# Optimization experiments

Measured on AMD Instinct MI355X. Metric: run time of the kernel, lower is better.

The kernel has to match this reference:

```python
import jax, jax.numpy as jnp
import numpy as np

DIM = 768
NUM_HEADS = 16
HEAD_DIM = DIM // NUM_HEADS
SCALE = HEAD_DIM ** -0.5


def setup_inputs() -> dict:
    key = jax.random.key(0)
    ks = jax.random.split(key, 9)
    B, S = 4, 2048
    init = 1.0 / np.sqrt(DIM)
    x = jax.random.normal(ks[0], (B, S, DIM), dtype=jnp.float32)
    Wq = jax.random.uniform(ks[1], (DIM, DIM), jnp.float32, -init, init)
    bq = jax.random.uniform(ks[2], (DIM,), jnp.float32, -init, init)
    Wk = jax.random.uniform(ks[3], (DIM, DIM), jnp.float32, -init, init)
    bk = jax.random.uniform(ks[4], (DIM,), jnp.float32, -init, init)
    Wv = jax.random.uniform(ks[5], (DIM, DIM), jnp.float32, -init, init)
    bv = jax.random.uniform(ks[6], (DIM,), jnp.float32, -init, init)
    Wo = jax.random.uniform(ks[7], (DIM, DIM), jnp.float32, -init, init)
    bo = jax.random.uniform(ks[8], (DIM,), jnp.float32, -init, init)
    return {"x": x, "Wq": Wq, "bq": bq, "Wk": Wk, "bk": bk,
            "Wv": Wv, "bv": bv, "Wo": Wo, "bo": bo}


def reference(x, Wq, bq, Wk, bk, Wv, bv, Wo, bo):
    B, S, D = x.shape
    H, Hd = NUM_HEADS, HEAD_DIM
    # Linear layers (torch Linear: y = x @ W^T + b); split heads -> [B,H,S,Hd]
    q = (x @ Wq.T + bq).reshape(B, S, H, Hd).transpose(0, 2, 1, 3)
    k = (x @ Wk.T + bk).reshape(B, S, H, Hd).transpose(0, 2, 1, 3)
    v = (x @ Wv.T + bv).reshape(B, S, H, Hd).transpose(0, 2, 1, 3)
    scores = jnp.einsum('bhqd,bhkd->bhqk', q, k) * SCALE  # [B,H,S,S]
    attn = jax.nn.softmax(scores, axis=-1)
    # dropout is identity in eval mode
    out = jnp.einsum('bhqk,bhkd->bhqd', attn, v)
    out = out.transpose(0, 2, 1, 3).reshape(B, S, D)
    return out @ Wo.T + bo
```

## Files before the change

kernel.cpp:

```cpp
#include <hip/hip_runtime.h>

typedef __bf16 bf16_t;
typedef bf16_t bf16x8 __attribute__((ext_vector_type(8)));
typedef _Float16 f16_t;
typedef __fp16 hf16x2 __attribute__((ext_vector_type(2)));
typedef f16_t f16x8 __attribute__((ext_vector_type(8)));
typedef float floatx4 __attribute__((ext_vector_type(4)));
typedef float floatx16 __attribute__((ext_vector_type(16)));

#define S_LEN 2048
#define DIM 768
#define NH 16
#define HD 48
#define HDP 64
#define BHEADS 64
#define ATT_SCALE 0.14433756729740643f
#define W_ELEMS (DIM * DIM)

typedef unsigned short u16;
typedef unsigned int u32;

__device__ __forceinline__ u16 f2b(float f) {
  union { float f; u32 i; } z; z.f = f;
  u32 i = z.i;
  return (u16)((i + 0x7fffu + ((i >> 16) & 1u)) >> 16);
}
__device__ __forceinline__ u32 pack2(float a, float b) {
  return (u32)f2b(a) | ((u32)f2b(b) << 16);
}
__device__ __forceinline__ u32 pkrtz2(float a, float b) {
  union { hf16x2 h; u32 u; } z;
  z.h = __builtin_amdgcn_cvt_pkrtz(a, b);
  return z.u;
}
__device__ __forceinline__ void pl32swap(u32& a, u32& b) {
  asm("v_permlane32_swap_b32 %0, %1" : "+v"(a), "+v"(b));
}

__global__ __launch_bounds__(256) void cvt_f32_bf16(
    const float* __restrict__ src, u16* __restrict__ dst)
{
  int idx = blockIdx.x * 256 + threadIdx.x;
  const float4* s = (const float4*)src;
  float4 a = s[idx * 2], b = s[idx * 2 + 1];
  *(uint4*)&dst[(size_t)idx * 8] =
      make_uint4(pack2(a.x, a.y), pack2(a.z, a.w), pack2(b.x, b.y), pack2(b.z, b.w));
}

__global__ __launch_bounds__(256) void cvt_weights(
    const float* __restrict__ w0, const float* __restrict__ w1,
    const float* __restrict__ w2, const float* __restrict__ w3,
    u16* __restrict__ dst)
{
  const float* srcs[4] = {w0, w1, w2, w3};
  const float* src = srcs[blockIdx.y];
  u16* d = dst + (size_t)blockIdx.y * W_ELEMS;
  int idx = blockIdx.x * 256 + threadIdx.x;
  const float4* s = (const float4*)src;
  float4 a = s[idx * 2], b = s[idx * 2 + 1];
  *(uint4*)&d[(size_t)idx * 8] =
      make_uint4(pack2(a.x, a.y), pack2(a.z, a.w), pack2(b.x, b.y), pack2(b.z, b.w));
}

template<int OMODE>
__global__ __launch_bounds__(256) void gemm_bt(
    const u16* __restrict__ A, const u16* __restrict__ W,
    const float* __restrict__ bias, void* __restrict__ outv, float scale)
{
  __shared__ __attribute__((aligned(16))) u16 smem[8704];
  u16 (*As)[40] = (u16(*)[40])smem;
  u16 (*Bs)[40] = (u16(*)[40])(smem + 5120);

  const int tid = threadIdx.x;
  const int w = tid >> 6, lane = tid & 63, lo = lane & 15, quad = lane >> 4;
  const int bm = blockIdx.x & 63, bn = blockIdx.x >> 6;
  const int m0 = bm * 128, n0 = bn * 64;

  floatx4 acc[2][4];
#pragma unroll
  for (int mi = 0; mi < 2; mi++)
#pragma unroll
    for (int ni = 0; ni < 4; ni++) acc[mi][ni] = (floatx4){0.f, 0.f, 0.f, 0.f};

  for (int k0 = 0; k0 < DIM; k0 += 32) {
#pragma unroll
    for (int it = 0; it < 2; ++it) {
      int c = tid + it * 256;
      int r = c >> 2, cc = c & 3;
      *(uint4*)&As[r][cc * 8] = *(const uint4*)&A[(size_t)(m0 + r) * DIM + k0 + cc * 8];
    }
    {
      int r = tid >> 2, cc = tid & 3;
      *(uint4*)&Bs[r][cc * 8] = *(const uint4*)&W[(size_t)(n0 + r) * DIM + k0 + cc * 8];
    }
    __syncthreads();
    bf16x8 af[2], bfr[4];
#pragma unroll
    for (int mi = 0; mi < 2; mi++) af[mi] = *(const bf16x8*)&As[w * 32 + mi * 16 + lo][quad * 8];
#pragma unroll
    for (int ni = 0; ni < 4; ni++) bfr[ni] = *(const bf16x8*)&Bs[ni * 16 + lo][quad * 8];
#pragma unroll
    for (int mi = 0; mi < 2; mi++)
#pragma unroll
      for (int ni = 0; ni < 4; ni++)
        acc[mi][ni] = __builtin_amdgcn_mfma_f32_16x16x32_bf16(af[mi], bfr[ni], acc[mi][ni], 0, 0, 0);
    __syncthreads();
  }

  if constexpr (OMODE == 2) {
    u16 (*T)[136] = (u16(*)[136])smem;
    u16* out = (u16*)outv;
#pragma unroll
    for (int mi = 0; mi < 2; mi++)
#pragma unroll
      for (int ni = 0; ni < 4; ni++) {
        int col = ni * 16 + lo;
        float bb = bias[n0 + col];
        float v0 = acc[mi][ni][0] + bb, v1 = acc[mi][ni][1] + bb;
        float v2 = acc[mi][ni][2] + bb, v3 = acc[mi][ni][3] + bb;
        *(uint2*)&T[col][w * 32 + mi * 16 + quad * 4] =
            make_uint2(pkrtz2(v0, v1), pkrtz2(v2, v3));
      }
    __syncthreads();
    const int b = m0 >> 11, s0 = m0 & 2047;
#pragma unroll
    for (int it = 0; it < 4; ++it) {
      int ch = tid + it * 256;
      int col = ch >> 4, sc = ch & 15;
      int gcol = n0 + col;
      int h = gcol / HD, d = gcol - h * HD;
      size_t dst = ((size_t)(b * NH + h) * HDP + d) * S_LEN + s0 + sc * 8;
      *(uint4*)&out[dst] = *(const uint4*)&T[col][sc * 8];
    }
    return;
  }

#pragma unroll
  for (int mi = 0; mi < 2; mi++)
#pragma unroll
    for (int ni = 0; ni < 4; ni++)
#pragma unroll
      for (int r = 0; r < 4; r++) {
        int row = m0 + w * 32 + mi * 16 + quad * 4 + r;
        int col = n0 + ni * 16 + lo;
        float v = (acc[mi][ni][r] + bias[col]) * scale;
        if constexpr (OMODE == 1) {
          ((float*)outv)[(size_t)row * DIM + col] = v;
        } else {
          int b = row >> 11, s = row & 2047;
          int h = col / HD, d = col - h * HD;
          ((u16*)outv)[((size_t)((b * NH + h) * S_LEN + s)) * HDP + d] = f2b(v);
        }
      }
}

#define STG_LOAD(k0n) do {                                                     \
  _Pragma("unroll")                                                            \
  for (int it = 0; it < 3; ++it) {                                             \
    int c = tid + it * 256;                                                    \
    if (c < 384) {                                                             \
      int r = c / 6, cc = c - r * 6;                                           \
      stg[it] = *(const uint4*)&K[base + (size_t)((k0n) + r) * HDP + cc * 8];  \
    } else {                                                                   \
      int c2 = c - 384, r = c2 >> 3, cc = c2 & 7;                              \
      stg[it] = *(const uint4*)&V[base + (size_t)r * S_LEN + (k0n) + cc * 8];  \
    }                                                                          \
  }                                                                            \
} while (0)

#define STG_WRITE(bufi) do {                                                   \
  _Pragma("unroll")                                                            \
  for (int it = 0; it < 3; ++it) {                                             \
    int c = tid + it * 256;                                                    \
    if (c < 384) {                                                             \
      int r = c / 6, cc = c - r * 6;                                           \
      *(uint4*)&Ks[bufi][r][cc * 8] = stg[it];                                 \
    } else {                                                                   \
      int c2 = c - 384, r = c2 >> 3, cc = c2 & 7;                              \
      *(uint4*)&Vt[bufi][r][cc * 8] = stg[it];                                 \
    }                                                                          \
  }                                                                            \
} while (0)

__global__ __launch_bounds__(256, 2) void attn_kernel(
    const u16* __restrict__ Q, const u16* __restrict__ K,
    const u16* __restrict__ V, u16* __restrict__ O)
{
  __shared__ __attribute__((aligned(16))) u16 Ks[2][64][56];
  __shared__ __attribute__((aligned(16))) u16 Vt[2][64][72];

  const int tid = threadIdx.x;
  const int w = tid >> 6, lane = tid & 63, l31 = lane & 31, hi = lane >> 5;
  const int q0 = blockIdx.x * 256;
  const int bh = blockIdx.y;
  const size_t base = (size_t)bh * S_LEN * HDP;

  bf16x8 qf[2][3];
#pragma unroll
  for (int t = 0; t < 2; t++)
#pragma unroll
    for (int ks = 0; ks < 3; ks++)
      qf[t][ks] = *(const bf16x8*)
          &Q[base + (size_t)(q0 + w * 64 + t * 32 + l31) * HDP + ks * 16 + hi * 8];

  floatx16 oacc[2][2];
#pragma unroll
  for (int t = 0; t < 2; t++)
#pragma unroll
    for (int nd = 0; nd < 2; nd++)
#pragma unroll
      for (int r = 0; r < 16; r++) oacc[t][nd][r] = 0.f;

  float l_lane[2] = {0.f, 0.f};

  uint4 stg[3];
  STG_LOAD(0);
  STG_WRITE(0);

  for (int ti = 0; ti < 32; ++ti) {
    const int cur = ti & 1;
    if (ti < 31) STG_LOAD((ti + 1) * 64);
    __syncthreads();

    bf16x8 ak[2][3];
#pragma unroll
    for (int na = 0; na < 2; na++)
#pragma unroll
      for (int ks = 0; ks < 3; ks++)
        ak[na][ks] = *(const bf16x8*)&Ks[cur][na * 32 + l31][ks * 16 + hi * 8];

    u32 pk[2][2][8];
#pragma unroll
    for (int t = 0; t < 2; t++) {
      floatx16 s0, s1;
#pragma unroll
      for (int r = 0; r < 16; r++) { s0[r] = 0.f; s1[r] = 0.f; }
#pragma unroll
      for (int ks = 0; ks < 3; ks++) {
        s0 = __builtin_amdgcn_mfma_f32_32x32x16_bf16(ak[0][ks], qf[t][ks], s0, 0, 0, 0);
        s1 = __builtin_amdgcn_mfma_f32_32x32x16_bf16(ak[1][ks], qf[t][ks], s1, 0, 0, 0);
      }
#pragma unroll
      for (int m = 0; m < 8; m++) {
        float a0 = __expf(s0[2 * m]), a1 = __expf(s0[2 * m + 1]);
        float b0 = __expf(s1[2 * m]), b1 = __expf(s1[2 * m + 1]);
        l_lane[t] += (a0 + a1) + (b0 + b1);
        pk[t][0][m] = pkrtz2(a0, a1);
        pk[t][1][m] = pkrtz2(b0, b1);
      }
    }

#pragma unroll
    for (int kt = 0; kt < 4; kt++) {
      f16x8 bv0 = *(const f16x8*)&Vt[cur][l31][kt * 16 + hi * 8];
      f16x8 bv1 = *(const f16x8*)&Vt[cur][32 + l31][kt * 16 + hi * 8];
      const int na = kt >> 1, k4 = (kt & 1) * 4;
#pragma unroll
      for (int t = 0; t < 2; t++) {
        u32 w0 = pk[t][na][k4 + 0], w2 = pk[t][na][k4 + 2];
        u32 w1 = pk[t][na][k4 + 1], w3 = pk[t][na][k4 + 3];
        pl32swap(w0, w2);
        pl32swap(w1, w3);
        union { u32 u[4]; f16x8 f; } af;
        af.u[0] = w0; af.u[1] = w1; af.u[2] = w2; af.u[3] = w3;
        oacc[t][0] = __builtin_amdgcn_mfma_f32_32x32x16_f16(af.f, bv0, oacc[t][0], 0, 0, 0);
        oacc[t][1] = __builtin_amdgcn_mfma_f32_32x32x16_f16(af.f, bv1, oacc[t][1], 0, 0, 0);
      }
    }

    if (ti < 31) STG_WRITE(cur ^ 1);
  }

  const int b = bh >> 4, h = bh & 15;
  float lt_full[2];
#pragma unroll
  for (int t = 0; t < 2; t++)
    lt_full[t] = l_lane[t] + __shfl_xor(l_lane[t], 32);
#pragma unroll
  for (int t = 0; t < 2; t++) {
#pragma unroll
    for (int r = 0; r < 16; r++) {
      int q_local = (r & 3) + 8 * (r >> 2) + 4 * hi;
      float l_r = __shfl(lt_full[t], q_local);
      float inv = 1.f / l_r;
      int q = q0 + w * 64 + t * 32 + q_local;
      size_t rowbase = ((size_t)(b * S_LEN + q)) * DIM + h * HD;
      O[rowbase + l31] = f2b(oacc[t][0][r] * inv);
      if (l31 < 16) O[rowbase + 32 + l31] = f2b(oacc[t][1][r] * inv);
    }
  }
}

extern "C" void kernel_launch(void* const* d_in, const int* in_sizes, int n_in,
                              void* d_out, int out_size, void* d_ws, size_t ws_size,
                              hipStream_t stream)
{
  const float* x  = (const float*)d_in[0];
  const float* Wq = (const float*)d_in[1];
  const float* bq = (const float*)d_in[2];
  const float* Wk = (const float*)d_in[3];
  const float* bk = (const float*)d_in[4];
  const float* Wv = (const float*)d_in[5];
  const float* bv = (const float*)d_in[6];
  const float* Wo = (const float*)d_in[7];
  const float* bo = (const float*)d_in[8];

  u16* ws   = (u16*)d_ws;
  const size_t qkv_elems = (size_t)BHEADS * S_LEN * HDP;
  u16* q_ws = ws;
  u16* k_ws = q_ws + qkv_elems;
  u16* v_ws = k_ws + qkv_elems;
  u16* x_bf = v_ws + qkv_elems;
  u16* a_ws = x_bf;
  u16* w_bf = x_bf + (size_t)8192 * DIM;

  cvt_f32_bf16<<<dim3(3072), dim3(256), 0, stream>>>(x, x_bf);
  cvt_weights<<<dim3(288, 4), dim3(256), 0, stream>>>(Wq, Wk, Wv, Wo, w_bf);
  u16* wq_bf = w_bf;
  u16* wk_bf = w_bf + (size_t)W_ELEMS;
  u16* wv_bf = w_bf + (size_t)2 * W_ELEMS;
  u16* wo_bf = w_bf + (size_t)3 * W_ELEMS;

  gemm_bt<0><<<dim3(768), dim3(256), 0, stream>>>(x_bf, wq_bf, bq, q_ws, ATT_SCALE);
  gemm_bt<0><<<dim3(768), dim3(256), 0, stream>>>(x_bf, wk_bf, bk, k_ws, 1.0f);
  gemm_bt<2><<<dim3(768), dim3(256), 0, stream>>>(x_bf, wv_bf, bv, v_ws, 1.0f);
  attn_kernel<<<dim3(S_LEN / 256, BHEADS), dim3(256), 0, stream>>>(q_ws, k_ws, v_ws, a_ws);
  gemm_bt<1><<<dim3(768), dim3(256), 0, stream>>>(a_ws, wo_bf, bo, d_out, 1.0f);
}
```

Measured before the change: 292.1 us.

## Halve attention query tile, raise occupancy, and remap blocks per XCD

Each attention block now handles 128 queries (32 per wave) instead of 256, so the grid grows from 512 to 1024 blocks and launch bounds move from 2 to 4 blocks per SM. A flat 1D grid is remapped so consecutive blocks on the same XCD share a head, which keeps that head's K/V in the XCD's L2. The aim is more concurrent waves to hide the exp/MFMA latency and better cache locality. The cost is twice as many K/V tile loads per query and less MFMA reuse of each K/V LDS fragment.

```diff
diff --git a/kernel.cpp b/kernel.cpp
--- a/kernel.cpp
+++ b/kernel.cpp
@@ -182,7 +182,7 @@
   }                                                                            \
 } while (0)
 
-__global__ __launch_bounds__(256, 2) void attn_kernel(
+__global__ __launch_bounds__(256, 4) void attn_kernel(
     const u16* __restrict__ Q, const u16* __restrict__ K,
     const u16* __restrict__ V, u16* __restrict__ O)
 {
@@ -191,27 +191,25 @@
 
   const int tid = threadIdx.x;
   const int w = tid >> 6, lane = tid & 63, l31 = lane & 31, hi = lane >> 5;
-  const int q0 = blockIdx.x * 256;
-  const int bh = blockIdx.y;
+  const int flat = blockIdx.x;
+  const int xcd = flat & 7, sub = flat >> 3;
+  const int bh = xcd * 8 + (sub >> 4);
+  const int q0 = (sub & 15) * 128;
   const size_t base = (size_t)bh * S_LEN * HDP;
 
-  bf16x8 qf[2][3];
-#pragma unroll
-  for (int t = 0; t < 2; t++)
-#pragma unroll
-    for (int ks = 0; ks < 3; ks++)
-      qf[t][ks] = *(const bf16x8*)
-          &Q[base + (size_t)(q0 + w * 64 + t * 32 + l31) * HDP + ks * 16 + hi * 8];
-
-  floatx16 oacc[2][2];
-#pragma unroll
-  for (int t = 0; t < 2; t++)
-#pragma unroll
-    for (int nd = 0; nd < 2; nd++)
-#pragma unroll
-      for (int r = 0; r < 16; r++) oacc[t][nd][r] = 0.f;
-
-  float l_lane[2] = {0.f, 0.f};
+  bf16x8 qf[3];
+#pragma unroll
+  for (int ks = 0; ks < 3; ks++)
+    qf[ks] = *(const bf16x8*)
+        &Q[base + (size_t)(q0 + w * 32 + l31) * HDP + ks * 16 + hi * 8];
+
+  floatx16 oacc[2];
+#pragma unroll
+  for (int nd = 0; nd < 2; nd++)
+#pragma unroll
+    for (int r = 0; r < 16; r++) oacc[nd][r] = 0.f;
+
+  float l_lane = 0.f;
 
   uint4 stg[3];
   STG_LOAD(0);
@@ -229,24 +227,23 @@
       for (int ks = 0; ks < 3; ks++)
         ak[na][ks] = *(const bf16x8*)&Ks[cur][na * 32 + l31][ks * 16 + hi * 8];
 
-    u32 pk[2][2][8];
-#pragma unroll
-    for (int t = 0; t < 2; t++) {
+    u32 pk[2][8];
+    {
       floatx16 s0, s1;
 #pragma unroll
       for (int r = 0; r < 16; r++) { s0[r] = 0.f; s1[r] = 0.f; }
 #pragma unroll
       for (int ks = 0; ks < 3; ks++) {
-        s0 = __builtin_amdgcn_mfma_f32_32x32x16_bf16(ak[0][ks], qf[t][ks], s0, 0, 0, 0);
-        s1 = __builtin_amdgcn_mfma_f32_32x32x16_bf16(ak[1][ks], qf[t][ks], s1, 0, 0, 0);
+        s0 = __builtin_amdgcn_mfma_f32_32x32x16_bf16(ak[0][ks], qf[ks], s0, 0, 0, 0);
+        s1 = __builtin_amdgcn_mfma_f32_32x32x16_bf16(ak[1][ks], qf[ks], s1, 0, 0, 0);
       }
 #pragma unroll
       for (int m = 0; m < 8; m++) {
         float a0 = __expf(s0[2 * m]), a1 = __expf(s0[2 * m + 1]);
         float b0 = __expf(s1[2 * m]), b1 = __expf(s1[2 * m + 1]);
-        l_lane[t] += (a0 + a1) + (b0 + b1);
-        pk[t][0][m] = pkrtz2(a0, a1);
-        pk[t][1][m] = pkrtz2(b0, b1);
+        l_lane += (a0 + a1) + (b0 + b1);
+        pk[0][m] = pkrtz2(a0, a1);
+        pk[1][m] = pkrtz2(b0, b1);
       }
     }
 
@@ -255,39 +252,30 @@
       f16x8 bv0 = *(const f16x8*)&Vt[cur][l31][kt * 16 + hi * 8];
       f16x8 bv1 = *(const f16x8*)&Vt[cur][32 + l31][kt * 16 + hi * 8];
       const int na = kt >> 1, k4 = (kt & 1) * 4;
-#pragma unroll
-      for (int t = 0; t < 2; t++) {
-        u32 w0 = pk[t][na][k4 + 0], w2 = pk[t][na][k4 + 2];
-        u32 w1 = pk[t][na][k4 + 1], w3 = pk[t][na][k4 + 3];
-        pl32swap(w0, w2);
-        pl32swap(w1, w3);
-        union { u32 u[4]; f16x8 f; } af;
-        af.u[0] = w0; af.u[1] = w1; af.u[2] = w2; af.u[3] = w3;
-        oacc[t][0] = __builtin_amdgcn_mfma_f32_32x32x16_f16(af.f, bv0, oacc[t][0], 0, 0, 0);
-        oacc[t][1] = __builtin_amdgcn_mfma_f32_32x32x16_f16(af.f, bv1, oacc[t][1], 0, 0, 0);
-      }
+      u32 w0 = pk[na][k4 + 0], w2 = pk[na][k4 + 2];
+      u32 w1 = pk[na][k4 + 1], w3 = pk[na][k4 + 3];
+      pl32swap(w0, w2);
+      pl32swap(w1, w3);
+      union { u32 u[4]; f16x8 f; } af;
+      af.u[0] = w0; af.u[1] = w1; af.u[2] = w2; af.u[3] = w3;
+      oacc[0] = __builtin_amdgcn_mfma_f32_32x32x16_f16(af.f, bv0, oacc[0], 0, 0, 0);
+      oacc[1] = __builtin_amdgcn_mfma_f32_32x32x16_f16(af.f, bv1, oacc[1], 0, 0, 0);
     }
 
     if (ti < 31) STG_WRITE(cur ^ 1);
   }
 
   const int b = bh >> 4, h = bh & 15;
-  float lt_full[2];
-#pragma unroll
-  for (int t = 0; t < 2; t++)
-    lt_full[t] = l_lane[t] + __shfl_xor(l_lane[t], 32);
-#pragma unroll
-  for (int t = 0; t < 2; t++) {
-#pragma unroll
-    for (int r = 0; r < 16; r++) {
-      int q_local = (r & 3) + 8 * (r >> 2) + 4 * hi;
-      float l_r = __shfl(lt_full[t], q_local);
-      float inv = 1.f / l_r;
-      int q = q0 + w * 64 + t * 32 + q_local;
-      size_t rowbase = ((size_t)(b * S_LEN + q)) * DIM + h * HD;
-      O[rowbase + l31] = f2b(oacc[t][0][r] * inv);
-      if (l31 < 16) O[rowbase + 32 + l31] = f2b(oacc[t][1][r] * inv);
-    }
+  float lt_full = l_lane + __shfl_xor(l_lane, 32);
+#pragma unroll
+  for (int r = 0; r < 16; r++) {
+    int q_local = (r & 3) + 8 * (r >> 2) + 4 * hi;
+    float l_r = __shfl(lt_full, q_local);
+    float inv = 1.f / l_r;
+    int q = q0 + w * 32 + q_local;
+    size_t rowbase = ((size_t)(b * S_LEN + q)) * DIM + h * HD;
+    O[rowbase + l31] = f2b(oacc[0][r] * inv);
+    if (l31 < 16) O[rowbase + 32 + l31] = f2b(oacc[1][r] * inv);
   }
 }
 
@@ -324,6 +312,6 @@
   gemm_bt<0><<<dim3(768), dim3(256), 0, stream>>>(x_bf, wq_bf, bq, q_ws, ATT_SCALE);
   gemm_bt<0><<<dim3(768), dim3(256), 0, stream>>>(x_bf, wk_bf, bk, k_ws, 1.0f);
   gemm_bt<2><<<dim3(768), dim3(256), 0, stream>>>(x_bf, wv_bf, bv, v_ws, 1.0f);
-  attn_kernel<<<dim3(S_LEN / 256, BHEADS), dim3(256), 0, stream>>>(q_ws, k_ws, v_ws, a_ws);
+  attn_kernel<<<dim3(1024), dim3(256), 0, stream>>>(q_ws, k_ws, v_ws, a_ws);
   gemm_bt<1><<<dim3(768), dim3(256), 0, stream>>>(a_ws, wo_bf, bo, d_out, 1.0f);
 }
```

New measurement: 299.9 us. 1.03x slower.
